# Kernel optimization log

Measured on AMD Instinct MI355X. Metric: run time of the kernel, lower is better.

Reference implementation:

```python
import jax, jax.numpy as jnp
import numpy as np

B, S, H = 1, 2048, 2048
NH, NKV, HD = 16, 4, 128
N_REP = NH // NKV
WINDOW = 1024
THETA = 10000.0


def _rope(x, fc):
    # x: [B,S,h,HD]; fc: [B,S,HD//2,2] (cos,sin)
    xr = x.reshape(*x.shape[:-1], HD // 2, 2)
    a, b = xr[..., 0], xr[..., 1]
    cos = fc[:, :, None, :, 0]
    sin = fc[:, :, None, :, 1]
    out = jnp.stack((a * cos - b * sin, a * sin + b * cos), axis=-1)
    return out.reshape(x.shape)


def setup_inputs() -> dict:
    key = jax.random.key(0)
    ks = jax.random.split(key, 5)
    hidden_state = jax.random.normal(ks[0], (B, S, H), jnp.float32)
    # rotary table: cos/sin of pos * theta^{-2i/d}
    inv_freq = 1.0 / (THETA ** (jnp.arange(0, HD, 2, dtype=jnp.float32) / HD))
    ang = jnp.arange(S, dtype=jnp.float32)[:, None] * inv_freq[None, :]  # [S, HD//2]
    freq_cis = jnp.stack((jnp.cos(ang), jnp.sin(ang)), axis=-1)  # [S, HD//2, 2]
    attention_mask = jnp.ones((B, S), dtype=bool)
    i = jnp.arange(S)[:, None]
    j = jnp.arange(S)[None, :]
    causal_mask = ((j <= i) & (i - j < WINDOW))[None, None]  # [1,1,S,S] sliding-window causal
    position_ids = jnp.broadcast_to(jnp.arange(S, dtype=jnp.int32), (B, S))
    scale = 0.02
    Wq = jax.random.normal(ks[1], (H, NH * HD), jnp.float32) * scale
    Wk = jax.random.normal(ks[2], (H, NKV * HD), jnp.float32) * scale
    Wv = jax.random.normal(ks[3], (H, NKV * HD), jnp.float32) * scale
    Wo = jax.random.normal(ks[4], (NH * HD, H), jnp.float32) * scale
    return {"hidden_state": hidden_state, "freq_cis": freq_cis,
            "attention_mask": attention_mask, "causal_mask": causal_mask,
            "position_ids": position_ids, "Wq": Wq, "Wk": Wk, "Wv": Wv, "Wo": Wo}


def reference(hidden_state, freq_cis, attention_mask, causal_mask, position_ids,
              Wq, Wk, Wv, Wo):
    q = (hidden_state @ Wq).reshape(B, S, NH, HD)
    k = (hidden_state @ Wk).reshape(B, S, NKV, HD)
    v = (hidden_state @ Wv).reshape(B, S, NKV, HD)
    fc = freq_cis[position_ids]  # [B,S,HD//2,2]
    q = _rope(q, fc)
    k = _rope(k, fc)
    # GQA: repeat kv heads (contiguous groups, as in repeat_kv)
    k = jnp.repeat(k, N_REP, axis=2)  # [B,S,NH,HD]
    v = jnp.repeat(v, N_REP, axis=2)
    mask = causal_mask & attention_mask[:, None, None, :]  # [B,1,S,S]
    bias = jnp.where(mask, 0.0, jnp.finfo(jnp.float32).min)
    scores = jnp.einsum('bqhd,bkhd->bhqk', q, k) * (1.0 / np.sqrt(HD))
    attn = jax.nn.softmax(scores + bias, axis=-1)
    out = jnp.einsum('bhqk,bkhd->bqhd', attn, v).reshape(B, S, NH * HD)
    return out @ Wo
```

## Files before the change

### kernel.cpp

```cpp
#include <hip/hip_runtime.h>
#include <hip/hip_bf16.h>
#include <stdint.h>

#define S_LEN 2048
#define HDIM  2048
#define NHQ   16
#define NKVH  4
#define HD    128
#define WIN   1024
#define SM_SCALE 0.08838834764831845f
#define NEG_BIG  -1.0e30f

typedef __attribute__((ext_vector_type(8))) short short8;
typedef __attribute__((ext_vector_type(4))) float float4v;
typedef unsigned short u16;

static __device__ __forceinline__ float bf2f(u16 u) {
  union { unsigned int i; float f; } v; v.i = ((unsigned int)u) << 16; return v.f;
}
static __device__ __forceinline__ u16 f2bf(float f) {
  union { float f; unsigned int i; } v; v.f = f;
  unsigned int x = v.i;
  return (u16)((x + 0x7fffu + ((x >> 16) & 1u)) >> 16);
}

__global__ __launch_bounds__(256) void prep(
    const float* __restrict__ hs, const float* __restrict__ Wq,
    const float* __restrict__ Wk, const float* __restrict__ Wv,
    const float* __restrict__ Wo, u16* __restrict__ hsB,
    u16* __restrict__ WqkvT, u16* __restrict__ WoT)
{
  const int b = blockIdx.x;
  if (b < 1024) {
    u16* dst = hsB + (size_t)b * 4096;
    const int mb = b >> 6, ks = b & 63;
#pragma unroll
    for (int i = 0; i < 2; ++i) {
      const int cid = i * 256 + threadIdx.x;
      const int kc  = cid & 3;
      const int m   = cid >> 2;
      const float* src = hs + ((size_t)(mb * 128 + m)) * 2048 + ks * 32 + kc * 8;
      const float4 v0 = *(const float4*)src;
      const float4 v1 = *(const float4*)(src + 4);
      short8 o;
      o[0] = (short)f2bf(v0.x); o[1] = (short)f2bf(v0.y);
      o[2] = (short)f2bf(v0.z); o[3] = (short)f2bf(v0.w);
      o[4] = (short)f2bf(v1.x); o[5] = (short)f2bf(v1.y);
      o[6] = (short)f2bf(v1.z); o[7] = (short)f2bf(v1.w);
      *(short8*)(dst + (kc * 128 + m) * 8) = o;
    }
    return;
  }

  __shared__ u16 t[32][33];
  const int tx = threadIdx.x & 31, ty = threadIdx.x >> 5;
  int n0, kstep;
  const float* W; u16* DT; int nsrc, N;
  if (b < 7168) {
    const int bb = b - 1024;
    n0    = (bb % 96) * 32;
    kstep = bb / 96;
    if (n0 < 2048)      { W = Wq; nsrc = n0;        N = 2048; }
    else if (n0 < 2560) { W = Wk; nsrc = n0 - 2048; N = 512;  }
    else                { W = Wv; nsrc = n0 - 2560; N = 512;  }
    DT = WqkvT;
  } else {
    const int bb = b - 7168;
    n0    = (bb & 63) * 32;
    kstep = bb >> 6;
    W = Wo; nsrc = n0; N = 2048; DT = WoT;
  }
  const int k0 = kstep * 32;

#pragma unroll
  for (int i = 0; i < 4; ++i)
    t[ty + i * 8][tx] = f2bf(W[(size_t)(k0 + ty + i * 8) * N + nsrc + tx]);
  __syncthreads();
  const int kc = tx >> 3, e = tx & 7;
#pragma unroll
  for (int i = 0; i < 4; ++i) {
    const int n = n0 + ty + i * 8;
    DT[((size_t)((n >> 6) * 64 + kstep)) * 2048 + kc * 512 + (n & 63) * 8 + e]
        = t[tx][ty + i * 8];
  }
}

template <int EPI>
__global__ __launch_bounds__(256) void gemm_bt(
    const u16* __restrict__ Apk, const u16* __restrict__ Bpk,
    void* __restrict__ Cv, const float* __restrict__ fc,
    u16* __restrict__ Qb, u16* __restrict__ Kp, u16* __restrict__ Vp,
    int M, int N, int K)
{
  __shared__ u16 Als[2][8192];
  __shared__ u16 Bls[2][4096];

  const int tid  = threadIdx.x;
  const int lane = tid & 63;
  const int w    = tid >> 6;
  const int quad = lane >> 4;
  const int lc   = lane & 15;
  const int n0   = blockIdx.x * 64;
  const int m0   = blockIdx.y * 128;
  const int wr   = (w >> 1) * 64;
  const int wc   = (w & 1) * 32;
  const int ktiles = K >> 5;
  const int nk2    = ktiles >> 1;

  const char* aB = (const char*)(Apk + (size_t)(m0 >> 7) * ktiles * 4096);
  const char* bB = (const char*)(Bpk + (size_t)(n0 >> 6) * ktiles * 2048);

  float4v acc[4][2];
#pragma unroll
  for (int i = 0; i < 4; ++i)
#pragma unroll
    for (int j = 0; j < 2; ++j) acc[i][j] = (float4v){0.f, 0.f, 0.f, 0.f};

  auto stage = [&](int bi, int kk) {
    const char* ab = aB + (size_t)kk * 16384;
    const char* bb = bB + (size_t)kk * 8192;
#pragma unroll
    for (int r = 0; r < 4; ++r) {
      const int off = r * 4096 + tid * 16;
      __builtin_amdgcn_global_load_lds(
          (__attribute__((address_space(1))) void*)(ab + off),
          (__attribute__((address_space(3))) void*)((char*)Als[bi] + off), 16, 0, 0);
    }
#pragma unroll
    for (int r = 0; r < 2; ++r) {
      const int off = r * 4096 + tid * 16;
      __builtin_amdgcn_global_load_lds(
          (__attribute__((address_space(1))) void*)(bb + off),
          (__attribute__((address_space(3))) void*)((char*)Bls[bi] + off), 16, 0, 0);
    }
  };

  stage(0, 0);
  __syncthreads();
  int cur = 0;
  for (int kk = 0; kk < nk2; ++kk) {
    if (kk + 1 < nk2) stage(cur ^ 1, kk + 1);
#pragma unroll
    for (int half = 0; half < 2; ++half) {
      const u16* Ab = Als[cur] + half * 4096;
      const u16* Bb = Bls[cur] + half * 2048;
      short8 af[4], bfr[2];
#pragma unroll
      for (int mi = 0; mi < 4; ++mi)
        af[mi] = *(const short8*)(Ab + quad * 1024 + (wr + mi * 16 + lc) * 8);
#pragma unroll
      for (int ni = 0; ni < 2; ++ni)
        bfr[ni] = *(const short8*)(Bb + quad * 512 + (wc + ni * 16 + lc) * 8);
#pragma unroll
      for (int mi = 0; mi < 4; ++mi)
#pragma unroll
        for (int ni = 0; ni < 2; ++ni)
          acc[mi][ni] = __builtin_amdgcn_mfma_f32_16x16x32_bf16(
              af[mi], bfr[ni], acc[mi][ni], 0, 0, 0);
    }
    __syncthreads();
    cur ^= 1;
  }

  if (EPI == 0) {
#pragma unroll
    for (int mi = 0; mi < 4; ++mi)
#pragma unroll
      for (int ni = 0; ni < 2; ++ni)
#pragma unroll
        for (int r = 0; r < 4; ++r) {
          const int row = m0 + wr + mi * 16 + quad * 4 + r;
          const int col = n0 + wc + ni * 16 + lc;
          ((float*)Cv)[(size_t)row * N + col] = acc[mi][ni][r];
        }
  } else {
    if (n0 < 2560) {
#pragma unroll
      for (int mi = 0; mi < 4; ++mi)
#pragma unroll
        for (int ni = 0; ni < 2; ++ni)
#pragma unroll
          for (int r = 0; r < 4; ++r) {
            const int row = m0 + wr + mi * 16 + quad * 4 + r;
            const int col = n0 + wc + ni * 16 + lc;
            const int hh  = col & 127;
            const float v = acc[mi][ni][r];
            const float p = __shfl_xor(v, 1);
            const float2 cs = *(const float2*)(fc + row * 128 + (hh & ~1));
            const float res = (col & 1) ? (p * cs.y + v * cs.x)
                                        : (v * cs.x - p * cs.y);
            if (n0 < 2048) {
              Qb[(size_t)row * 2048 + col] = f2bf(res);
            } else {
              const int kvh = (col - 2048) >> 7;
              const int kt  = row >> 6, key = row & 63;
              const int ks   = hh >> 5;
              const int qd   = (hh >> 3) & 3;
              const int e    = hh & 7;
              const int ntk  = key >> 4;
              const int lck  = key & 15;
              Kp[((size_t)(kvh * 32 + kt)) * 8192
                 + ((ks * 4 + ntk) << 9) + ((qd * 16 + lck) << 3) + e] = f2bf(res);
            }
          }
    } else {
#pragma unroll
      for (int mi = 0; mi < 4; ++mi)
#pragma unroll
        for (int ni = 0; ni < 2; ++ni)
#pragma unroll
          for (int r = 0; r < 4; ++r) {
            const int row = m0 + wr + mi * 16 + quad * 4 + r;
            const int col = n0 + wc + ni * 16 + lc;
            const int kvh = (col - 2560) >> 7;
            const int hd  = col & 127;
            const int kt  = row >> 6, key = row & 63;
            const int ktk  = (key >> 5) & 1;
            const int qd   = (key >> 3) & 3;
            const int e    = key & 7;
            const int nt2  = hd >> 4;
            const int lcv  = hd & 15;
            Vp[((size_t)(kvh * 32 + kt)) * 8192
               + ((ktk * 8 + nt2) << 9) + ((qd * 16 + lcv) << 3) + e]
                = f2bf(acc[mi][ni][r]);
          }
    }
  }
}

__global__ __launch_bounds__(64, 2) void attn_kernel(
    const u16* __restrict__ Qb, const u16* __restrict__ kp,
    const u16* __restrict__ vp, u16* __restrict__ out)
{
  __shared__ u16 P[16 * 72];

  const int lane = threadIdx.x;
  const int quad = lane >> 4;
  const int lc   = lane & 15;

  const int id = blockIdx.x;
  const int u  = id & 255;
  const int g  = id >> 8;
  const int h  = u & 15;
  const int w  = (u >> 4) & 3;
  const int j2 = u >> 6;
  const int t  = g * 4 + j2;
  const int kvh = h >> 2;
  const int rb  = t * 64 + w * 16;

  short8 qf[4];
  {
    const u16* qp = Qb + (size_t)(rb + lc) * 2048 + h * HD + quad * 8;
#pragma unroll
    for (int ks = 0; ks < 4; ++ks) qf[ks] = *(const short8*)(qp + ks * 32);
  }

  float4v o[8];
#pragma unroll
  for (int i = 0; i < 8; ++i) o[i] = (float4v){0.f, 0.f, 0.f, 0.f};
  float mrow[4], lrow[4];
#pragma unroll
  for (int r = 0; r < 4; ++r) { mrow[r] = NEG_BIG; lrow[r] = 0.f; }

  int jmin = rb - (WIN - 1); if (jmin < 0) jmin = 0;
  const int kt_begin = jmin >> 6;
  const int kt_end   = (rb + 15) >> 6;

  const size_t tbase = (size_t)(kvh * 32) * 8192;
  const int lofs = lane << 3;

  short8 ka[8], kb8[8];
  {
    const u16* kg = kp + tbase + (size_t)kt_begin * 8192;
#pragma unroll
    for (int i = 0; i < 8; ++i) ka[i]  = *(const short8*)(kg + (i << 9) + lofs);
#pragma unroll
    for (int i = 0; i < 8; ++i) kb8[i] = *(const short8*)(kg + ((8 + i) << 9) + lofs);
  }

  for (int kt = kt_begin; kt <= kt_end; ++kt) {
    const int k0 = kt * 64;

    short8 va[8], vb8[8];
    {
      const u16* vg = vp + tbase + (size_t)kt * 8192;
#pragma unroll
      for (int i = 0; i < 8; ++i) va[i]  = *(const short8*)(vg + (i << 9) + lofs);
#pragma unroll
      for (int i = 0; i < 8; ++i) vb8[i] = *(const short8*)(vg + ((8 + i) << 9) + lofs);
    }

    float4v sacc[4];
#pragma unroll
    for (int i = 0; i < 4; ++i) sacc[i] = (float4v){0.f, 0.f, 0.f, 0.f};
    __builtin_amdgcn_s_setprio(1);
#pragma unroll
    for (int nt = 0; nt < 4; ++nt) {
      sacc[nt] = __builtin_amdgcn_mfma_f32_16x16x32_bf16(qf[0], ka[nt],      sacc[nt], 0, 0, 0);
      sacc[nt] = __builtin_amdgcn_mfma_f32_16x16x32_bf16(qf[1], ka[4 + nt],  sacc[nt], 0, 0, 0);
      sacc[nt] = __builtin_amdgcn_mfma_f32_16x16x32_bf16(qf[2], kb8[nt],     sacc[nt], 0, 0, 0);
      sacc[nt] = __builtin_amdgcn_mfma_f32_16x16x32_bf16(qf[3], kb8[4 + nt], sacc[nt], 0, 0, 0);
    }
    __builtin_amdgcn_s_setprio(0);

    if (kt < kt_end) {
      const u16* kg = kp + tbase + (size_t)(kt + 1) * 8192;
#pragma unroll
      for (int i = 0; i < 8; ++i) ka[i]  = *(const short8*)(kg + (i << 9) + lofs);
#pragma unroll
      for (int i = 0; i < 8; ++i) kb8[i] = *(const short8*)(kg + ((8 + i) << 9) + lofs);
    }

    const bool full = (k0 + 63 <= rb) && ((rb + 15 - k0) <= WIN - 1);
    float rmax[4] = {NEG_BIG, NEG_BIG, NEG_BIG, NEG_BIG};
    if (full) {
#pragma unroll
      for (int nt = 0; nt < 4; ++nt)
#pragma unroll
        for (int r = 0; r < 4; ++r) {
          const float sx = sacc[nt][r] * SM_SCALE;
          sacc[nt][r] = sx;
          rmax[r] = fmaxf(rmax[r], sx);
        }
    } else {
#pragma unroll
      for (int nt = 0; nt < 4; ++nt) {
        const int j = k0 + nt * 16 + lc;
#pragma unroll
        for (int r = 0; r < 4; ++r) {
          const int i = rb + quad * 4 + r;
          const bool valid = (j <= i) && (i - j < WIN);
          const float sx = valid ? sacc[nt][r] * SM_SCALE : NEG_BIG;
          sacc[nt][r] = sx;
          rmax[r] = fmaxf(rmax[r], sx);
        }
      }
    }
#pragma unroll
    for (int off = 1; off < 16; off <<= 1)
#pragma unroll
      for (int r = 0; r < 4; ++r)
        rmax[r] = fmaxf(rmax[r], __shfl_xor(rmax[r], off, 64));

    bool grow = false;
#pragma unroll
    for (int r = 0; r < 4; ++r) grow |= (rmax[r] > mrow[r]);
    if (__any((int)grow)) {
#pragma unroll
      for (int r = 0; r < 4; ++r) {
        const float mn = fmaxf(mrow[r], rmax[r]);
        const float a  = __expf(mrow[r] - mn);
        mrow[r] = mn;
        lrow[r] *= a;
#pragma unroll
        for (int i = 0; i < 8; ++i) o[i][r] *= a;
      }
    }

    float rsum[4] = {0.f, 0.f, 0.f, 0.f};
#pragma unroll
    for (int nt = 0; nt < 4; ++nt)
#pragma unroll
      for (int r = 0; r < 4; ++r) {
        const float p = __expf(sacc[nt][r] - mrow[r]);
        rsum[r] += p;
        P[(quad * 4 + r) * 72 + nt * 16 + lc] = f2bf(p);
      }
#pragma unroll
    for (int off = 1; off < 16; off <<= 1)
#pragma unroll
      for (int r = 0; r < 4; ++r)
        rsum[r] += __shfl_xor(rsum[r], off, 64);
#pragma unroll
    for (int r = 0; r < 4; ++r) lrow[r] += rsum[r];

    __builtin_amdgcn_s_setprio(1);
    {
      short8 pa0 = *(const short8*)(P + lc * 72 + quad * 8);
#pragma unroll
      for (int nt2 = 0; nt2 < 8; ++nt2)
        o[nt2] = __builtin_amdgcn_mfma_f32_16x16x32_bf16(pa0, va[nt2], o[nt2], 0, 0, 0);
      short8 pa1 = *(const short8*)(P + lc * 72 + 32 + quad * 8);
#pragma unroll
      for (int nt2 = 0; nt2 < 8; ++nt2)
        o[nt2] = __builtin_amdgcn_mfma_f32_16x16x32_bf16(pa1, vb8[nt2], o[nt2], 0, 0, 0);
    }
    __builtin_amdgcn_s_setprio(0);
  }

#pragma unroll
  for (int r = 0; r < 4; ++r) {
    const float inv = (lrow[r] > 0.f) ? (1.f / lrow[r]) : 0.f;
    const int row = rb + quad * 4 + r;
    const size_t mbase = (size_t)(row >> 7) * 64;
    const int m = row & 127;
#pragma unroll
    for (int nt2 = 0; nt2 < 8; ++nt2) {
      const int col = h * HD + nt2 * 16 + lc;
      const int kstep = col >> 5, kc = (col >> 3) & 3, e = col & 7;
      out[(mbase + kstep) * 4096 + kc * 1024 + m * 8 + e] = f2bf(o[nt2][r] * inv);
    }
  }
}

extern "C" void kernel_launch(void* const* d_in, const int* in_sizes, int n_in,
                              void* d_out, int out_size, void* d_ws, size_t ws_size,
                              hipStream_t stream) {
  const float* hs = (const float*)d_in[0];
  const float* fc = (const float*)d_in[1];
  const float* Wq = (const float*)d_in[5];
  const float* Wk = (const float*)d_in[6];
  const float* Wv = (const float*)d_in[7];
  const float* Wo = (const float*)d_in[8];
  float* outp = (float*)d_out;

  u16* hsB   = (u16*)d_ws;
  u16* WqkvT = hsB   + (size_t)2048 * 2048;
  u16* WoT   = WqkvT + (size_t)3072 * 2048;
  u16* Qb    = WoT   + (size_t)2048 * 2048;
  u16* ATTN  = Qb    + (size_t)2048 * 2048;
  u16* Kp    = ATTN  + (size_t)2048 * 2048;
  u16* Vp    = Kp    + (size_t)4 * 2048 * 128;

  dim3 blk(256);
  prep<<<dim3(11264), blk, 0, stream>>>(hs, Wq, Wk, Wv, Wo, hsB, WqkvT, WoT);
  gemm_bt<1><<<dim3(3072 / 64, 2048 / 128), blk, 0, stream>>>(
      hsB, WqkvT, nullptr, fc, Qb, Kp, Vp, 2048, 3072, 2048);
  attn_kernel<<<dim3(2048), dim3(64), 0, stream>>>(Qb, Kp, Vp, ATTN);
  gemm_bt<0><<<dim3(2048 / 64, 2048 / 128), blk, 0, stream>>>(
      ATTN, WoT, outp, nullptr, nullptr, nullptr, nullptr, 2048, 2048, 2048);
}
```

Baseline: 224.9 us.

## Split attention key range across two blocks and merge with a combine kernel

Each query tile's key range is split into two halves, each handled by its own block, which doubles the attention grid. Each block writes an unnormalized bf16 partial output plus its running row max and row sum. A new combine kernel rescales and merges the two partials into the final attention layout. The occupancy hint also rises from 2 to 4 waves, and the partials reuse the already-consumed input-cast workspace. The aim is more parallelism to fill the GPU, at the cost of an extra launch, extra global traffic for the partials, and some bf16 rounding of unnormalized partial outputs.

```diff
diff --git a/kernel.cpp b/kernel.cpp
--- a/kernel.cpp
+++ b/kernel.cpp
@@ -228,19 +228,19 @@
   }
 }
 
-__global__ __launch_bounds__(64, 2) void attn_kernel(
+__global__ __launch_bounds__(64, 4) void attn_kernel(
     const u16* __restrict__ Qb, const u16* __restrict__ kp,
-    const u16* __restrict__ vp, u16* __restrict__ out)
+    const u16* __restrict__ vp, u16* __restrict__ PART, float* __restrict__ ML)
 {
-  __shared__ u16 P[16 * 72];
-
   const int lane = threadIdx.x;
   const int quad = lane >> 4;
   const int lc   = lane & 15;
 
   const int id = blockIdx.x;
   const int u  = id & 255;
-  const int g  = id >> 8;
+  const int g2 = id >> 8;
+  const int s  = g2 >> 3;
+  const int g  = g2 & 7;
   const int h  = u & 15;
   const int w  = (u >> 4) & 3;
   const int j2 = u >> 6;
@@ -265,20 +265,25 @@
   int jmin = rb - (WIN - 1); if (jmin < 0) jmin = 0;
   const int kt_begin = jmin >> 6;
   const int kt_end   = (rb + 15) >> 6;
+  const int ntile    = kt_end - kt_begin + 1;
+  const int nhalf    = (ntile + 1) >> 1;
+  const int my_begin = (s == 0) ? kt_begin : kt_begin + nhalf;
+  const int my_end   = (s == 0) ? kt_begin + nhalf - 1 : kt_end;
 
   const size_t tbase = (size_t)(kvh * 32) * 8192;
   const int lofs = lane << 3;
 
+  const int ktp = (my_begin <= 31) ? my_begin : 31;
   short8 ka[8], kb8[8];
   {
-    const u16* kg = kp + tbase + (size_t)kt_begin * 8192;
+    const u16* kg = kp + tbase + (size_t)ktp * 8192;
 #pragma unroll
     for (int i = 0; i < 8; ++i) ka[i]  = *(const short8*)(kg + (i << 9) + lofs);
 #pragma unroll
     for (int i = 0; i < 8; ++i) kb8[i] = *(const short8*)(kg + ((8 + i) << 9) + lofs);
   }
 
-  for (int kt = kt_begin; kt <= kt_end; ++kt) {
+  for (int kt = my_begin; kt <= my_end; ++kt) {
     const int k0 = kt * 64;
 
     short8 va[8], vb8[8];
@@ -303,7 +308,7 @@
     }
     __builtin_amdgcn_s_setprio(0);
 
-    if (kt < kt_end) {
+    if (kt < my_end) {
       const u16* kg = kp + tbase + (size_t)(kt + 1) * 8192;
 #pragma unroll
       for (int i = 0; i < 8; ++i) ka[i]  = *(const short8*)(kg + (i << 9) + lofs);
@@ -357,6 +362,7 @@
       }
     }
 
+    __shared__ u16 P[16 * 72];
     float rsum[4] = {0.f, 0.f, 0.f, 0.f};
 #pragma unroll
     for (int nt = 0; nt < 4; ++nt)
@@ -390,16 +396,57 @@
 
 #pragma unroll
   for (int r = 0; r < 4; ++r) {
-    const float inv = (lrow[r] > 0.f) ? (1.f / lrow[r]) : 0.f;
-    const int row = rb + quad * 4 + r;
-    const size_t mbase = (size_t)(row >> 7) * 64;
-    const int m = row & 127;
-#pragma unroll
-    for (int nt2 = 0; nt2 < 8; ++nt2) {
-      const int col = h * HD + nt2 * 16 + lc;
-      const int kstep = col >> 5, kc = (col >> 3) & 3, e = col & 7;
-      out[(mbase + kstep) * 4096 + kc * 1024 + m * 8 + e] = f2bf(o[nt2][r] * inv);
-    }
+    const int lr = quad * 4 + r;
+#pragma unroll
+    for (int nt2 = 0; nt2 < 8; ++nt2)
+      PART[(size_t)id * 2048 + lr * 128 + nt2 * 16 + lc] = f2bf(o[nt2][r]);
+    if (lc == 0)
+      *(float2*)(ML + (size_t)id * 32 + lr * 2) = make_float2(mrow[r], lrow[r]);
+  }
+}
+
+__global__ __launch_bounds__(256) void combine_kernel(
+    const u16* __restrict__ PART, const float* __restrict__ ML,
+    u16* __restrict__ out)
+{
+  const int tid  = threadIdx.x;
+  const int lane = tid & 63;
+  const int grp  = blockIdx.x * 4 + (tid >> 6);
+  const int u    = grp & 255;
+  const int g    = grp >> 8;
+  const int h    = u & 15;
+  const int w    = (u >> 4) & 3;
+  const int j2   = u >> 6;
+  const int t    = g * 4 + j2;
+
+  const int row16 = lane >> 2;
+  const int cq    = lane & 3;
+
+  const size_t id0 = grp, id1 = grp + 2048;
+  const float2 ml0 = *(const float2*)(ML + id0 * 32 + row16 * 2);
+  const float2 ml1 = *(const float2*)(ML + id1 * 32 + row16 * 2);
+  const float m  = fmaxf(ml0.x, ml1.x);
+  const float a0 = __expf(ml0.x - m), a1 = __expf(ml1.x - m);
+  const float l  = a0 * ml0.y + a1 * ml1.y;
+  const float inv = (l > 0.f) ? 1.f / l : 0.f;
+  const float f0 = a0 * inv, f1 = a1 * inv;
+
+  const int row   = t * 64 + w * 16 + row16;
+  const size_t mbase = (size_t)(row >> 7) * 64;
+  const int mloc  = row & 127;
+  const int kstep = h * 4 + cq;
+
+  const u16* p0 = PART + id0 * 2048 + row16 * 128 + cq * 32;
+  const u16* p1 = PART + id1 * 2048 + row16 * 128 + cq * 32;
+#pragma unroll
+  for (int j = 0; j < 4; ++j) {
+    short8 a = *(const short8*)(p0 + j * 8);
+    short8 b = *(const short8*)(p1 + j * 8);
+    short8 ov;
+#pragma unroll
+    for (int e = 0; e < 8; ++e)
+      ov[e] = (short)f2bf(bf2f((u16)a[e]) * f0 + bf2f((u16)b[e]) * f1);
+    *(short8*)(out + (mbase + kstep) * 4096 + j * 1024 + mloc * 8) = ov;
   }
 }
 
@@ -422,11 +469,15 @@
   u16* Kp    = ATTN  + (size_t)2048 * 2048;
   u16* Vp    = Kp    + (size_t)4 * 2048 * 128;
 
+  u16*   PARTb = hsB;
+  float* MLf   = (float*)(hsB + (size_t)4096 * 2048);
+
   dim3 blk(256);
   prep<<<dim3(11264), blk, 0, stream>>>(hs, Wq, Wk, Wv, Wo, hsB, WqkvT, WoT);
   gemm_bt<1><<<dim3(3072 / 64, 2048 / 128), blk, 0, stream>>>(
       hsB, WqkvT, nullptr, fc, Qb, Kp, Vp, 2048, 3072, 2048);
-  attn_kernel<<<dim3(2048), dim3(64), 0, stream>>>(Qb, Kp, Vp, ATTN);
+  attn_kernel<<<dim3(4096), dim3(64), 0, stream>>>(Qb, Kp, Vp, PARTb, MLf);
+  combine_kernel<<<dim3(512), blk, 0, stream>>>(PARTb, MLf, ATTN);
   gemm_bt<0><<<dim3(2048 / 64, 2048 / 128), blk, 0, stream>>>(
       ATTN, WoT, outp, nullptr, nullptr, nullptr, nullptr, 2048, 2048, 2048);
 }
```

Measured after the change: 446.5 us. 1.99x slower.

## Process two 16-row query tiles per attention wave to reuse K/V loads

Applied to the files above, without the earlier changes.

Each single-wave attention block now handles 32 query rows (two 16-row MFMA tiles) instead of 16, so every K and V tile loaded from global memory feeds twice as many MFMAs. The grid is halved to 1024 blocks and the block-to-(head, row) mapping is simplified. This cuts K/V global traffic per query row. In exchange it roughly doubles accumulator and Q-fragment registers, which may reduce occupancy under launch_bounds(64,2), and leaves fewer blocks to spread across CUs.

```diff
diff --git a/kernel.cpp b/kernel.cpp
--- a/kernel.cpp
+++ b/kernel.cpp
@@ -232,39 +232,41 @@
     const u16* __restrict__ Qb, const u16* __restrict__ kp,
     const u16* __restrict__ vp, u16* __restrict__ out)
 {
-  __shared__ u16 P[16 * 72];
+  __shared__ u16 P[2][16 * 72];
 
   const int lane = threadIdx.x;
   const int quad = lane >> 4;
   const int lc   = lane & 15;
 
   const int id = blockIdx.x;
-  const int u  = id & 255;
-  const int g  = id >> 8;
-  const int h  = u & 15;
-  const int w  = (u >> 4) & 3;
-  const int j2 = u >> 6;
-  const int t  = g * 4 + j2;
+  const int h  = id & 15;
+  const int w2 = (id >> 4) & 1;
+  const int t  = id >> 5;
   const int kvh = h >> 2;
-  const int rb  = t * 64 + w * 16;
-
-  short8 qf[4];
-  {
-    const u16* qp = Qb + (size_t)(rb + lc) * 2048 + h * HD + quad * 8;
-#pragma unroll
-    for (int ks = 0; ks < 4; ++ks) qf[ks] = *(const short8*)(qp + ks * 32);
-  }
-
-  float4v o[8];
-#pragma unroll
-  for (int i = 0; i < 8; ++i) o[i] = (float4v){0.f, 0.f, 0.f, 0.f};
-  float mrow[4], lrow[4];
-#pragma unroll
-  for (int r = 0; r < 4; ++r) { mrow[r] = NEG_BIG; lrow[r] = 0.f; }
+  const int rb  = t * 64 + w2 * 32;
+
+  short8 qf[2][4];
+#pragma unroll
+  for (int mt = 0; mt < 2; ++mt) {
+    const u16* qp = Qb + (size_t)(rb + mt * 16 + lc) * 2048 + h * HD + quad * 8;
+#pragma unroll
+    for (int ks = 0; ks < 4; ++ks) qf[mt][ks] = *(const short8*)(qp + ks * 32);
+  }
+
+  float4v o[2][8];
+#pragma unroll
+  for (int mt = 0; mt < 2; ++mt)
+#pragma unroll
+    for (int i = 0; i < 8; ++i) o[mt][i] = (float4v){0.f, 0.f, 0.f, 0.f};
+  float mrow[2][4], lrow[2][4];
+#pragma unroll
+  for (int mt = 0; mt < 2; ++mt)
+#pragma unroll
+    for (int r = 0; r < 4; ++r) { mrow[mt][r] = NEG_BIG; lrow[mt][r] = 0.f; }
 
   int jmin = rb - (WIN - 1); if (jmin < 0) jmin = 0;
   const int kt_begin = jmin >> 6;
-  const int kt_end   = (rb + 15) >> 6;
+  const int kt_end   = (rb + 31) >> 6;
 
   const size_t tbase = (size_t)(kvh * 32) * 8192;
   const int lofs = lane << 3;
@@ -290,17 +292,21 @@
       for (int i = 0; i < 8; ++i) vb8[i] = *(const short8*)(vg + ((8 + i) << 9) + lofs);
     }
 
-    float4v sacc[4];
-#pragma unroll
-    for (int i = 0; i < 4; ++i) sacc[i] = (float4v){0.f, 0.f, 0.f, 0.f};
+    float4v sacc[2][4];
+#pragma unroll
+    for (int mt = 0; mt < 2; ++mt)
+#pragma unroll
+      for (int i = 0; i < 4; ++i) sacc[mt][i] = (float4v){0.f, 0.f, 0.f, 0.f};
     __builtin_amdgcn_s_setprio(1);
 #pragma unroll
-    for (int nt = 0; nt < 4; ++nt) {
-      sacc[nt] = __builtin_amdgcn_mfma_f32_16x16x32_bf16(qf[0], ka[nt],      sacc[nt], 0, 0, 0);
-      sacc[nt] = __builtin_amdgcn_mfma_f32_16x16x32_bf16(qf[1], ka[4 + nt],  sacc[nt], 0, 0, 0);
-      sacc[nt] = __builtin_amdgcn_mfma_f32_16x16x32_bf16(qf[2], kb8[nt],     sacc[nt], 0, 0, 0);
-      sacc[nt] = __builtin_amdgcn_mfma_f32_16x16x32_bf16(qf[3], kb8[4 + nt], sacc[nt], 0, 0, 0);
-    }
+    for (int mt = 0; mt < 2; ++mt)
+#pragma unroll
+      for (int nt = 0; nt < 4; ++nt) {
+        sacc[mt][nt] = __builtin_amdgcn_mfma_f32_16x16x32_bf16(qf[mt][0], ka[nt],      sacc[mt][nt], 0, 0, 0);
+        sacc[mt][nt] = __builtin_amdgcn_mfma_f32_16x16x32_bf16(qf[mt][1], ka[4 + nt],  sacc[mt][nt], 0, 0, 0);
+        sacc[mt][nt] = __builtin_amdgcn_mfma_f32_16x16x32_bf16(qf[mt][2], kb8[nt],     sacc[mt][nt], 0, 0, 0);
+        sacc[mt][nt] = __builtin_amdgcn_mfma_f32_16x16x32_bf16(qf[mt][3], kb8[4 + nt], sacc[mt][nt], 0, 0, 0);
+      }
     __builtin_amdgcn_s_setprio(0);
 
     if (kt < kt_end) {
@@ -311,96 +317,120 @@
       for (int i = 0; i < 8; ++i) kb8[i] = *(const short8*)(kg + ((8 + i) << 9) + lofs);
     }
 
-    const bool full = (k0 + 63 <= rb) && ((rb + 15 - k0) <= WIN - 1);
-    float rmax[4] = {NEG_BIG, NEG_BIG, NEG_BIG, NEG_BIG};
-    if (full) {
-#pragma unroll
-      for (int nt = 0; nt < 4; ++nt)
-#pragma unroll
-        for (int r = 0; r < 4; ++r) {
-          const float sx = sacc[nt][r] * SM_SCALE;
-          sacc[nt][r] = sx;
-          rmax[r] = fmaxf(rmax[r], sx);
-        }
-    } else {
-#pragma unroll
-      for (int nt = 0; nt < 4; ++nt) {
-        const int j = k0 + nt * 16 + lc;
-#pragma unroll
-        for (int r = 0; r < 4; ++r) {
-          const int i = rb + quad * 4 + r;
-          const bool valid = (j <= i) && (i - j < WIN);
-          const float sx = valid ? sacc[nt][r] * SM_SCALE : NEG_BIG;
-          sacc[nt][r] = sx;
-          rmax[r] = fmaxf(rmax[r], sx);
+    float rmax[2][4];
+#pragma unroll
+    for (int mt = 0; mt < 2; ++mt) {
+      const int rbm = rb + mt * 16;
+      const bool full = (k0 + 63 <= rbm) && ((rbm + 15 - k0) <= WIN - 1);
+#pragma unroll
+      for (int r = 0; r < 4; ++r) rmax[mt][r] = NEG_BIG;
+      if (full) {
+#pragma unroll
+        for (int nt = 0; nt < 4; ++nt)
+#pragma unroll
+          for (int r = 0; r < 4; ++r) {
+            const float sx = sacc[mt][nt][r] * SM_SCALE;
+            sacc[mt][nt][r] = sx;
+            rmax[mt][r] = fmaxf(rmax[mt][r], sx);
+          }
+      } else {
+#pragma unroll
+        for (int nt = 0; nt < 4; ++nt) {
+          const int j = k0 + nt * 16 + lc;
+#pragma unroll
+          for (int r = 0; r < 4; ++r) {
+            const int i = rbm + quad * 4 + r;
+            const bool valid = (j <= i) && (i - j < WIN);
+            const float sx = valid ? sacc[mt][nt][r] * SM_SCALE : NEG_BIG;
+            sacc[mt][nt][r] = sx;
+            rmax[mt][r] = fmaxf(rmax[mt][r], sx);
+          }
         }
       }
     }
 #pragma unroll
     for (int off = 1; off < 16; off <<= 1)
 #pragma unroll
-      for (int r = 0; r < 4; ++r)
-        rmax[r] = fmaxf(rmax[r], __shfl_xor(rmax[r], off, 64));
+      for (int mt = 0; mt < 2; ++mt)
+#pragma unroll
+        for (int r = 0; r < 4; ++r)
+          rmax[mt][r] = fmaxf(rmax[mt][r], __shfl_xor(rmax[mt][r], off, 64));
 
     bool grow = false;
 #pragma unroll
-    for (int r = 0; r < 4; ++r) grow |= (rmax[r] > mrow[r]);
+    for (int mt = 0; mt < 2; ++mt)
+#pragma unroll
+      for (int r = 0; r < 4; ++r) grow |= (rmax[mt][r] > mrow[mt][r]);
     if (__any((int)grow)) {
 #pragma unroll
-      for (int r = 0; r < 4; ++r) {
-        const float mn = fmaxf(mrow[r], rmax[r]);
-        const float a  = __expf(mrow[r] - mn);
-        mrow[r] = mn;
-        lrow[r] *= a;
-#pragma unroll
-        for (int i = 0; i < 8; ++i) o[i][r] *= a;
+      for (int mt = 0; mt < 2; ++mt)
+#pragma unroll
+        for (int r = 0; r < 4; ++r) {
+          const float mn = fmaxf(mrow[mt][r], rmax[mt][r]);
+          const float a  = __expf(mrow[mt][r] - mn);
+          mrow[mt][r] = mn;
+          lrow[mt][r] *= a;
+#pragma unroll
+          for (int i = 0; i < 8; ++i) o[mt][i][r] *= a;
+        }
+    }
+
+    float rsum[2][4];
+#pragma unroll
+    for (int mt = 0; mt < 2; ++mt) {
+#pragma unroll
+      for (int r = 0; r < 4; ++r) rsum[mt][r] = 0.f;
+#pragma unroll
+      for (int nt = 0; nt < 4; ++nt)
+#pragma unroll
+        for (int r = 0; r < 4; ++r) {
+          const float p = __expf(sacc[mt][nt][r] - mrow[mt][r]);
+          rsum[mt][r] += p;
+          P[mt][(quad * 4 + r) * 72 + nt * 16 + lc] = f2bf(p);
+        }
+    }
+#pragma unroll
+    for (int off = 1; off < 16; off <<= 1)
+#pragma unroll
+      for (int mt = 0; mt < 2; ++mt)
+#pragma unroll
+        for (int r = 0; r < 4; ++r)
+          rsum[mt][r] += __shfl_xor(rsum[mt][r], off, 64);
+#pragma unroll
+    for (int mt = 0; mt < 2; ++mt)
+#pragma unroll
+      for (int r = 0; r < 4; ++r) lrow[mt][r] += rsum[mt][r];
+
+    __builtin_amdgcn_s_setprio(1);
+#pragma unroll
+    for (int mt = 0; mt < 2; ++mt) {
+      short8 pa0 = *(const short8*)(P[mt] + lc * 72 + quad * 8);
+#pragma unroll
+      for (int nt2 = 0; nt2 < 8; ++nt2)
+        o[mt][nt2] = __builtin_amdgcn_mfma_f32_16x16x32_bf16(pa0, va[nt2], o[mt][nt2], 0, 0, 0);
+      short8 pa1 = *(const short8*)(P[mt] + lc * 72 + 32 + quad * 8);
+#pragma unroll
+      for (int nt2 = 0; nt2 < 8; ++nt2)
+        o[mt][nt2] = __builtin_amdgcn_mfma_f32_16x16x32_bf16(pa1, vb8[nt2], o[mt][nt2], 0, 0, 0);
+    }
+    __builtin_amdgcn_s_setprio(0);
+  }
+
+#pragma unroll
+  for (int mt = 0; mt < 2; ++mt)
+#pragma unroll
+    for (int r = 0; r < 4; ++r) {
+      const float inv = (lrow[mt][r] > 0.f) ? (1.f / lrow[mt][r]) : 0.f;
+      const int row = rb + mt * 16 + quad * 4 + r;
+      const size_t mbase = (size_t)(row >> 7) * 64;
+      const int m = row & 127;
+#pragma unroll
+      for (int nt2 = 0; nt2 < 8; ++nt2) {
+        const int col = h * HD + nt2 * 16 + lc;
+        const int kstep = col >> 5, kc = (col >> 3) & 3, e = col & 7;
+        out[(mbase + kstep) * 4096 + kc * 1024 + m * 8 + e] = f2bf(o[mt][nt2][r] * inv);
       }
     }
-
-    float rsum[4] = {0.f, 0.f, 0.f, 0.f};
-#pragma unroll
-    for (int nt = 0; nt < 4; ++nt)
-#pragma unroll
-      for (int r = 0; r < 4; ++r) {
-        const float p = __expf(sacc[nt][r] - mrow[r]);
-        rsum[r] += p;
-        P[(quad * 4 + r) * 72 + nt * 16 + lc] = f2bf(p);
-      }
-#pragma unroll
-    for (int off = 1; off < 16; off <<= 1)
-#pragma unroll
-      for (int r = 0; r < 4; ++r)
-        rsum[r] += __shfl_xor(rsum[r], off, 64);
-#pragma unroll
-    for (int r = 0; r < 4; ++r) lrow[r] += rsum[r];
-
-    __builtin_amdgcn_s_setprio(1);
-    {
-      short8 pa0 = *(const short8*)(P + lc * 72 + quad * 8);
-#pragma unroll
-      for (int nt2 = 0; nt2 < 8; ++nt2)
-        o[nt2] = __builtin_amdgcn_mfma_f32_16x16x32_bf16(pa0, va[nt2], o[nt2], 0, 0, 0);
-      short8 pa1 = *(const short8*)(P + lc * 72 + 32 + quad * 8);
-#pragma unroll
-      for (int nt2 = 0; nt2 < 8; ++nt2)
-        o[nt2] = __builtin_amdgcn_mfma_f32_16x16x32_bf16(pa1, vb8[nt2], o[nt2], 0, 0, 0);
-    }
-    __builtin_amdgcn_s_setprio(0);
-  }
-
-#pragma unroll
-  for (int r = 0; r < 4; ++r) {
-    const float inv = (lrow[r] > 0.f) ? (1.f / lrow[r]) : 0.f;
-    const int row = rb + quad * 4 + r;
-    const size_t mbase = (size_t)(row >> 7) * 64;
-    const int m = row & 127;
-#pragma unroll
-    for (int nt2 = 0; nt2 < 8; ++nt2) {
-      const int col = h * HD + nt2 * 16 + lc;
-      const int kstep = col >> 5, kc = (col >> 3) & 3, e = col & 7;
-      out[(mbase + kstep) * 4096 + kc * 1024 + m * 8 + e] = f2bf(o[nt2][r] * inv);
-    }
-  }
 }
 
 extern "C" void kernel_launch(void* const* d_in, const int* in_sizes, int n_in,
@@ -426,7 +456,7 @@
   prep<<<dim3(11264), blk, 0, stream>>>(hs, Wq, Wk, Wv, Wo, hsB, WqkvT, WoT);
   gemm_bt<1><<<dim3(3072 / 64, 2048 / 128), blk, 0, stream>>>(
       hsB, WqkvT, nullptr, fc, Qb, Kp, Vp, 2048, 3072, 2048);
-  attn_kernel<<<dim3(2048), dim3(64), 0, stream>>>(Qb, Kp, Vp, ATTN);
+  attn_kernel<<<dim3(1024), dim3(64), 0, stream>>>(Qb, Kp, Vp, ATTN);
   gemm_bt<0><<<dim3(2048 / 64, 2048 / 128), blk, 0, stream>>>(
       ATTN, WoT, outp, nullptr, nullptr, nullptr, nullptr, 2048, 2048, 2048);
 }
```

Measured after the change: 326.8 us. +45.4%, slower.
